# Kernel tuning notes

Hardware: AMD Instinct MI355X
Metric: run time of the kernel (lower is better)

## Reference

```python
import jax, jax.numpy as jnp
import numpy as np

BITS = 8
EPS = 1e-5


def round_clip(x, lo, hi):
    # round-then-clip with straight-through estimator (matches Audyn's round_clip)
    return x + jax.lax.stop_gradient(jnp.clip(jnp.round(x), lo, hi) - x)


def setup_inputs() -> dict:
    key = jax.random.key(0)
    kx, kw = jax.random.split(key)
    B, S, D_IN, D_OUT = 4, 2048, 4096, 16384
    x = jax.random.normal(kx, (B, S, D_IN), dtype=jnp.float32)
    # kaiming-uniform-ish scale: bound = 1/sqrt(in_features)
    bound = 1.0 / np.sqrt(D_IN)
    weight = jax.random.uniform(kw, (D_OUT, D_IN), dtype=jnp.float32,
                                minval=-bound, maxval=bound)
    return {"x": x, "weight": weight}


def reference(x, weight):
    q = float(2 ** (BITS - 1))  # 128
    # activation quantization: per-tensor abs-max
    gamma = jnp.maximum(jnp.max(jnp.abs(x)), EPS)
    xq = round_clip(x * (q / gamma), -q, q - 1.0)
    # weight quantization: per-tensor mean-abs (NB: source divides abs_weight, not weight)
    abs_w = jnp.abs(weight)
    beta = jnp.maximum(jnp.mean(abs_w), EPS)
    wq = round_clip(abs_w / beta, -1.0, 1.0)
    # GEMM (no bias: source always registers bias as None) + rescale
    y = jnp.einsum("bsd,od->bso", xq, wq)
    return y * (beta * gamma / q)
```

## Files before the change

kernel.cpp:

```cpp
#include <hip/hip_runtime.h>

typedef float f32x4 __attribute__((ext_vector_type(4)));
typedef int   i32x4 __attribute__((ext_vector_type(4)));
typedef char  s8x16 __attribute__((ext_vector_type(16)));

#define GAS __attribute__((address_space(1)))
#define LAS __attribute__((address_space(3)))

constexpr int M = 8192;
constexpr int N = 16384;
constexpr int K = 4096;
constexpr long long NX = (long long)M * K;
constexpr long long NW = (long long)N * K;
constexpr int NPART = 2048;

constexpr int BKB    = 64;
constexpr int NTT    = K / BKB;
constexpr int ABYTES = 256 * BKB;
constexpr int BBYTES = 128 * BKB;
constexpr int BUFB   = ABYTES + BBYTES;


__global__ void reduce_absmax_kernel(const float* __restrict__ x,
                                     unsigned* __restrict__ gmax, int n4) {
  float m = 0.f;
  int stride = gridDim.x * blockDim.x;
  for (int i = blockIdx.x * blockDim.x + threadIdx.x; i < n4; i += stride) {
    f32x4 v = *(const f32x4*)(x + (size_t)i * 4);
    m = fmaxf(m, fmaxf(fmaxf(fabsf(v[0]), fabsf(v[1])),
                       fmaxf(fabsf(v[2]), fabsf(v[3]))));
  }
#pragma unroll
  for (int off = 32; off > 0; off >>= 1) m = fmaxf(m, __shfl_down(m, off));
  __shared__ float sm[4];
  int lane = threadIdx.x & 63, wid = threadIdx.x >> 6;
  if (lane == 0) sm[wid] = m;
  __syncthreads();
  if (threadIdx.x == 0) {
    m = fmaxf(fmaxf(sm[0], sm[1]), fmaxf(sm[2], sm[3]));
    atomicMax(gmax, __float_as_uint(m));
  }
}

__global__ void reduce_abssum_kernel(const float* __restrict__ w,
                                     float* __restrict__ partials, int n4) {
  float s = 0.f;
  int stride = gridDim.x * blockDim.x;
  for (int i = blockIdx.x * blockDim.x + threadIdx.x; i < n4; i += stride) {
    f32x4 v = *(const f32x4*)(w + (size_t)i * 4);
    s += fabsf(v[0]) + fabsf(v[1]) + fabsf(v[2]) + fabsf(v[3]);
  }
#pragma unroll
  for (int off = 32; off > 0; off >>= 1) s += __shfl_down(s, off);
  __shared__ float sm[4];
  int lane = threadIdx.x & 63, wid = threadIdx.x >> 6;
  if (lane == 0) sm[wid] = s;
  __syncthreads();
  if (threadIdx.x == 0) partials[blockIdx.x] = (sm[0] + sm[1]) + (sm[2] + sm[3]);
}

__global__ void finalize_kernel(const unsigned* __restrict__ gbits,
                                const float* __restrict__ partials,
                                float* __restrict__ params) {
  __shared__ double sd[256];
  double s = 0.0;
  for (int i = threadIdx.x; i < NPART; i += 256) s += (double)partials[i];
  sd[threadIdx.x] = s;
  __syncthreads();
  for (int h = 128; h > 0; h >>= 1) {
    if (threadIdx.x < h) sd[threadIdx.x] += sd[threadIdx.x + h];
    __syncthreads();
  }
  if (threadIdx.x == 0) {
    float beta  = fmaxf((float)(sd[0] / (double)NW), 1e-5f);
    float gamma = fmaxf(__uint_as_float(gbits[0]), 1e-5f);
    params[0] = 128.0f / gamma;
    params[1] = beta;
    params[2] = beta * gamma / 128.0f;
  }
}


__global__ void quant_x_kernel(const float* __restrict__ x,
                               char* __restrict__ xq,
                               const float* __restrict__ params, int n16) {
  float s = params[0];
  int stride = gridDim.x * blockDim.x;
  for (int i = blockIdx.x * blockDim.x + threadIdx.x; i < n16; i += stride) {
    const f32x4* p = (const f32x4*)(x + (size_t)i * 16);
    s8x16 o;
#pragma unroll
    for (int v = 0; v < 4; ++v) {
      f32x4 t = p[v];
#pragma unroll
      for (int k = 0; k < 4; ++k) {
        float r = fminf(fmaxf(rintf(t[k] * s), -128.f), 127.f);
        o[v * 4 + k] = (char)(int)r;
      }
    }
    *(s8x16*)(xq + (size_t)i * 16) = o;
  }
}

__global__ void quant_w_kernel(const float* __restrict__ w,
                               char* __restrict__ wq,
                               const float* __restrict__ params, int n16) {
  float beta = params[1];
  int stride = gridDim.x * blockDim.x;
  for (int i = blockIdx.x * blockDim.x + threadIdx.x; i < n16; i += stride) {
    const f32x4* p = (const f32x4*)(w + (size_t)i * 16);
    s8x16 o;
#pragma unroll
    for (int v = 0; v < 4; ++v) {
      f32x4 t = p[v];
#pragma unroll
      for (int k = 0; k < 4; ++k) {
        o[v * 4 + k] = (rintf(fabsf(t[k]) / beta) >= 1.0f) ? (char)1 : (char)0;
      }
    }
    *(s8x16*)(wq + (size_t)i * 16) = o;
  }
}


__global__ __launch_bounds__(512, 4) void gemm_kernel(
    const char* __restrict__ A,
    const char* __restrict__ B,
    float* __restrict__ C,
    const float* __restrict__ params) {
  __shared__ __align__(16) char lds[3 * BUFB];

  const int tid  = threadIdx.x;
  const int lane = tid & 63, wid = tid >> 6;
  const int wm = wid >> 1, wn = wid & 1;
  const int r16 = lane & 15, q4 = lane >> 4;

  const int wg = (blockIdx.x & 7) * 512 + (blockIdx.x >> 3);
  const int m0 = (wg >> 7) * 256, n0 = (wg & 127) * 128;

  const int csw = (((lane & 3) ^ ((lane >> 3) & 3))) * 16;
  const char* gA = A + (size_t)(m0 + wid * 32 + (lane >> 2)) * K + csw;
  const char* gB = B + (size_t)(n0 + wid * 16 + (lane >> 2)) * K + csw;
  const int dA = wid * 2048 + lane * 16;
  const int dB = ABYTES + wid * 1024 + lane * 16;

  auto stage = [&](int t, int bo) {
    char* L = lds + bo;
    const char* a = gA + t * BKB;
    __builtin_amdgcn_global_load_lds((const GAS void*)a,              (LAS void*)(L + dA),        16, 0, 0);
    __builtin_amdgcn_global_load_lds((const GAS void*)(a + 16 * K),   (LAS void*)(L + dA + 1024), 16, 0, 0);
    __builtin_amdgcn_global_load_lds((const GAS void*)(gB + t * BKB), (LAS void*)(L + dB),        16, 0, 0);
  };

  int aoff[4], boff[4];
  const int rsw = ((q4 ^ ((r16 >> 1) & 3)) * 16);
#pragma unroll
  for (int i = 0; i < 4; ++i)
    aoff[i] = (wm * 64 + i * 16 + r16) * BKB + rsw;
#pragma unroll
  for (int j = 0; j < 4; ++j)
    boff[j] = ABYTES + (wn * 64 + j * 16 + r16) * BKB + rsw;

  i32x4 acc[4][4] = {};

  auto compute = [&](int bo) {
    const char* buf = lds + bo;
    i32x4 af[4], bf[4];
#pragma unroll
    for (int i = 0; i < 4; ++i) af[i] = *(const i32x4*)(buf + aoff[i]);
#pragma unroll
    for (int j = 0; j < 4; ++j) bf[j] = *(const i32x4*)(buf + boff[j]);
    __builtin_amdgcn_s_setprio(1);
#pragma unroll
    for (int i = 0; i < 4; ++i)
#pragma unroll
      for (int j = 0; j < 4; ++j)
        acc[i][j] = __builtin_amdgcn_mfma_i32_16x16x64_i8(af[i], bf[j], acc[i][j], 0, 0, 0);
    __builtin_amdgcn_s_setprio(0);
  };

  stage(0, 0);
  stage(1, BUFB);

  int cb = 0, sb = 2 * BUFB;
  for (int t = 0; t < NTT - 1; ++t) {
    asm volatile("s_waitcnt vmcnt(3)" ::: "memory");
    __builtin_amdgcn_sched_barrier(0);
    __builtin_amdgcn_s_barrier();
    __builtin_amdgcn_sched_barrier(0);
    if (t + 2 < NTT) stage(t + 2, sb);
    compute(cb);
    cb = (cb == 2 * BUFB) ? 0 : cb + BUFB;
    sb = (sb == 2 * BUFB) ? 0 : sb + BUFB;
  }
  asm volatile("s_waitcnt vmcnt(0)" ::: "memory");
  __builtin_amdgcn_sched_barrier(0);
  __builtin_amdgcn_s_barrier();
  __builtin_amdgcn_sched_barrier(0);
  compute(cb);

  const float sc = params[2];
  const int crow = m0 + wm * 64 + q4 * 4;
  const int ccol = n0 + wn * 64 + r16;
#pragma unroll
  for (int i = 0; i < 4; ++i)
#pragma unroll
    for (int j = 0; j < 4; ++j)
#pragma unroll
      for (int r = 0; r < 4; ++r)
        C[(size_t)(crow + i * 16 + r) * N + (ccol + j * 16)] = (float)acc[i][j][r] * sc;
}


extern "C" void kernel_launch(void* const* d_in, const int* in_sizes, int n_in,
                              void* d_out, int out_size, void* d_ws, size_t ws_size,
                              hipStream_t stream) {
  const float* x = (const float*)d_in[0];
  const float* w = (const float*)d_in[1];
  float* out = (float*)d_out;
  char* ws = (char*)d_ws;

  unsigned* gamma_bits = (unsigned*)ws;
  float*    params     = (float*)(ws + 16);
  float*    partials   = (float*)(ws + 256);
  char*     xq = ws + 16384;
  char*     wq = ws + 16384 + (size_t)NX;

  hipMemsetAsync(ws, 0, 256, stream);

  reduce_absmax_kernel<<<NPART, 256, 0, stream>>>(x, gamma_bits, (int)(NX / 4));
  reduce_abssum_kernel<<<NPART, 256, 0, stream>>>(w, partials, (int)(NW / 4));
  finalize_kernel<<<1, 256, 0, stream>>>(gamma_bits, partials, params);
  quant_x_kernel<<<2048, 256, 0, stream>>>(x, xq, params, (int)(NX / 16));
  quant_w_kernel<<<2048, 256, 0, stream>>>(w, wq, params, (int)(NW / 16));

  gemm_kernel<<<4096, 512, 0, stream>>>(xq, wq, out, params);
}
```

Before: 756.3 us.

## Swap GEMM tile to 128x256 with 256 threads and 4x8 fragments per wave

The int8 GEMM block goes from 512 threads on a 256x128 tile to 256 threads on a 128x256 tile. Each wave now computes a 64x128 output with 4x8 MFMA fragments instead of 4x4. The aim is higher MFMA-to-LDS-read reuse per wave and fewer waves sharing the barrier, with tile order remapped along N. The cost is more accumulator registers per thread (128 VGPRs of accumulators), lower occupancy, and six async loads per stage instead of three.

Result: slower. 884.6 us (+17.0%).

```diff
diff --git a/kernel.cpp b/kernel.cpp
--- a/kernel.cpp
+++ b/kernel.cpp
@@ -1,11 +1,12 @@
 #include <hip/hip_runtime.h>
 
-typedef float f32x4 __attribute__((ext_vector_type(4)));
-typedef int   i32x4 __attribute__((ext_vector_type(4)));
-typedef char  s8x16 __attribute__((ext_vector_type(16)));
+typedef float f32x4  __attribute__((ext_vector_type(4)));
+typedef int   i32x4  __attribute__((ext_vector_type(4)));
+typedef char  s8x16  __attribute__((ext_vector_type(16)));
 
 #define GAS __attribute__((address_space(1)))
 #define LAS __attribute__((address_space(3)))
+#define SBAR __builtin_amdgcn_sched_barrier(0)
 
 constexpr int M = 8192;
 constexpr int N = 16384;
@@ -14,11 +15,11 @@
 constexpr long long NW = (long long)N * K;
 constexpr int NPART = 2048;
 
-constexpr int BKB    = 64;
-constexpr int NTT    = K / BKB;
-constexpr int ABYTES = 256 * BKB;
-constexpr int BBYTES = 128 * BKB;
-constexpr int BUFB   = ABYTES + BBYTES;
+constexpr int BKB  = 64;
+constexpr int NTT  = K / BKB;
+constexpr int ABY  = 128 * BKB;
+constexpr int BBY  = 256 * BKB;
+constexpr int BUFB = ABY + BBY;
 
 
 __global__ void reduce_absmax_kernel(const float* __restrict__ x,
@@ -123,7 +124,7 @@
 }
 
 
-__global__ __launch_bounds__(512, 4) void gemm_kernel(
+__global__ __launch_bounds__(256, 2) void gemm_kernel(
     const char* __restrict__ A,
     const char* __restrict__ B,
     float* __restrict__ C,
@@ -131,51 +132,55 @@
   __shared__ __align__(16) char lds[3 * BUFB];
 
   const int tid  = threadIdx.x;
-  const int lane = tid & 63, wid = tid >> 6;
+  const int lane = tid & 63;
+  const int wid  = tid >> 6;
   const int wm = wid >> 1, wn = wid & 1;
   const int r16 = lane & 15, q4 = lane >> 4;
 
   const int wg = (blockIdx.x & 7) * 512 + (blockIdx.x >> 3);
-  const int m0 = (wg >> 7) * 256, n0 = (wg & 127) * 128;
-
-  const int csw = (((lane & 3) ^ ((lane >> 3) & 3))) * 16;
-  const char* gA = A + (size_t)(m0 + wid * 32 + (lane >> 2)) * K + csw;
-  const char* gB = B + (size_t)(n0 + wid * 16 + (lane >> 2)) * K + csw;
-  const int dA = wid * 2048 + lane * 16;
-  const int dB = ABYTES + wid * 1024 + lane * 16;
+  const int m0 = (wg & 63) * 128;
+  const int n0 = (wg >> 6) * 256;
+
+  const int csw = ((tid & 3) ^ ((tid >> 3) & 3)) * 16;
+  const char* gA = A + (size_t)(m0 + (tid >> 2)) * K + csw;
+  const char* gB = B + (size_t)(n0 + (tid >> 2)) * K + csw;
+  const int dst = tid * 16;
 
   auto stage = [&](int t, int bo) {
     char* L = lds + bo;
-    const char* a = gA + t * BKB;
-    __builtin_amdgcn_global_load_lds((const GAS void*)a,              (LAS void*)(L + dA),        16, 0, 0);
-    __builtin_amdgcn_global_load_lds((const GAS void*)(a + 16 * K),   (LAS void*)(L + dA + 1024), 16, 0, 0);
-    __builtin_amdgcn_global_load_lds((const GAS void*)(gB + t * BKB), (LAS void*)(L + dB),        16, 0, 0);
+    const size_t ko = (size_t)t * BKB;
+    __builtin_amdgcn_global_load_lds((const GAS void*)(gA + ko),                (LAS void*)(L + dst),         16, 0, 0);
+    __builtin_amdgcn_global_load_lds((const GAS void*)(gA + ko + (size_t)64*K), (LAS void*)(L + 4096 + dst),  16, 0, 0);
+    __builtin_amdgcn_global_load_lds((const GAS void*)(gB + ko),                (LAS void*)(L + ABY + dst),          16, 0, 0);
+    __builtin_amdgcn_global_load_lds((const GAS void*)(gB + ko + (size_t)64*K), (LAS void*)(L + ABY + 4096 + dst),   16, 0, 0);
+    __builtin_amdgcn_global_load_lds((const GAS void*)(gB + ko + (size_t)128*K),(LAS void*)(L + ABY + 8192 + dst),   16, 0, 0);
+    __builtin_amdgcn_global_load_lds((const GAS void*)(gB + ko + (size_t)192*K),(LAS void*)(L + ABY + 12288 + dst),  16, 0, 0);
   };
 
-  int aoff[4], boff[4];
   const int rsw = ((q4 ^ ((r16 >> 1) & 3)) * 16);
-#pragma unroll
-  for (int i = 0; i < 4; ++i)
-    aoff[i] = (wm * 64 + i * 16 + r16) * BKB + rsw;
-#pragma unroll
-  for (int j = 0; j < 4; ++j)
-    boff[j] = ABYTES + (wn * 64 + j * 16 + r16) * BKB + rsw;
-
-  i32x4 acc[4][4] = {};
+  int aoff[4], boff[8];
+#pragma unroll
+  for (int fm = 0; fm < 4; ++fm)
+    aoff[fm] = (wm * 64 + fm * 16 + r16) * BKB + rsw;
+#pragma unroll
+  for (int fn = 0; fn < 8; ++fn)
+    boff[fn] = ABY + (wn * 128 + fn * 16 + r16) * BKB + rsw;
+
+  i32x4 acc[4][8] = {};
 
   auto compute = [&](int bo) {
     const char* buf = lds + bo;
-    i32x4 af[4], bf[4];
-#pragma unroll
-    for (int i = 0; i < 4; ++i) af[i] = *(const i32x4*)(buf + aoff[i]);
-#pragma unroll
-    for (int j = 0; j < 4; ++j) bf[j] = *(const i32x4*)(buf + boff[j]);
+    i32x4 af[4], bf[8];
+#pragma unroll
+    for (int fm = 0; fm < 4; ++fm) af[fm] = *(const i32x4*)(buf + aoff[fm]);
+#pragma unroll
+    for (int fn = 0; fn < 8; ++fn) bf[fn] = *(const i32x4*)(buf + boff[fn]);
     __builtin_amdgcn_s_setprio(1);
 #pragma unroll
-    for (int i = 0; i < 4; ++i)
-#pragma unroll
-      for (int j = 0; j < 4; ++j)
-        acc[i][j] = __builtin_amdgcn_mfma_i32_16x16x64_i8(af[i], bf[j], acc[i][j], 0, 0, 0);
+    for (int fn = 0; fn < 8; ++fn)
+#pragma unroll
+      for (int fm = 0; fm < 4; ++fm)
+        acc[fm][fn] = __builtin_amdgcn_mfma_i32_16x16x64_i8(af[fm], bf[fn], acc[fm][fn], 0, 0, 0);
     __builtin_amdgcn_s_setprio(0);
   };
 
@@ -183,32 +188,31 @@
   stage(1, BUFB);
 
   int cb = 0, sb = 2 * BUFB;
-  for (int t = 0; t < NTT - 1; ++t) {
-    asm volatile("s_waitcnt vmcnt(3)" ::: "memory");
-    __builtin_amdgcn_sched_barrier(0);
+  for (int t = 0; t < NTT; ++t) {
+    if (t < NTT - 1) {
+      asm volatile("s_waitcnt vmcnt(6)" ::: "memory");
+    } else {
+      asm volatile("s_waitcnt vmcnt(0)" ::: "memory");
+    }
+    SBAR;
     __builtin_amdgcn_s_barrier();
-    __builtin_amdgcn_sched_barrier(0);
+    SBAR;
     if (t + 2 < NTT) stage(t + 2, sb);
     compute(cb);
     cb = (cb == 2 * BUFB) ? 0 : cb + BUFB;
     sb = (sb == 2 * BUFB) ? 0 : sb + BUFB;
   }
-  asm volatile("s_waitcnt vmcnt(0)" ::: "memory");
-  __builtin_amdgcn_sched_barrier(0);
-  __builtin_amdgcn_s_barrier();
-  __builtin_amdgcn_sched_barrier(0);
-  compute(cb);
 
   const float sc = params[2];
   const int crow = m0 + wm * 64 + q4 * 4;
-  const int ccol = n0 + wn * 64 + r16;
-#pragma unroll
-  for (int i = 0; i < 4; ++i)
-#pragma unroll
-    for (int j = 0; j < 4; ++j)
+  const int ccol = n0 + wn * 128 + r16;
+#pragma unroll
+  for (int fm = 0; fm < 4; ++fm)
+#pragma unroll
+    for (int fn = 0; fn < 8; ++fn)
 #pragma unroll
       for (int r = 0; r < 4; ++r)
-        C[(size_t)(crow + i * 16 + r) * N + (ccol + j * 16)] = (float)acc[i][j][r] * sc;
+        C[(size_t)(crow + fm * 16 + r) * N + (ccol + fn * 16)] = (float)acc[fm][fn][r] * sc;
 }
 
 
@@ -234,5 +238,5 @@
   quant_x_kernel<<<2048, 256, 0, stream>>>(x, xq, params, (int)(NX / 16));
   quant_w_kernel<<<2048, 256, 0, stream>>>(w, wq, params, (int)(NW / 16));
 
-  gemm_kernel<<<4096, 512, 0, stream>>>(xq, wq, out, params);
-}
+  gemm_kernel<<<4096, 256, 0, stream>>>(xq, wq, out, params);
+}
```
